# Optimization experiments

Measured on AMD Instinct MI355X. Metric: run time of the kernel, lower is better.

Reference implementation:

```python
import jax, jax.numpy as jnp
import numpy as np

D_MODEL = 1024
NHEADS = 16
E_HEAD = D_MODEL // NHEADS  # 64
ROPE_BASE = 10000.0


def _rope_cos_sin(L, dim, base, dtype):
    # dim = E_head (even); inv_freq over pairs, GPT-NeoX half-split convention
    inv_freq = 1.0 / (base ** (jnp.arange(0, dim, 2, dtype=jnp.float32) / dim))
    pos = jnp.arange(L, dtype=jnp.float32)
    freqs = pos[:, None] * inv_freq[None, :]  # [L, dim/2]
    return jnp.cos(freqs).astype(dtype), jnp.sin(freqs).astype(dtype)


def _apply_rope(t, cos, sin):
    # t: [B, H, L, Dh]; rotate-half formulation
    d2 = t.shape[-1] // 2
    t1, t2 = t[..., :d2], t[..., d2:]
    return jnp.concatenate([t1 * cos - t2 * sin, t1 * sin + t2 * cos], axis=-1)


def setup_inputs() -> dict:
    key = jax.random.key(0)
    ks = jax.random.split(key, 5)
    B, L = 4, 2048
    x = jax.random.normal(ks[0], (B, L, D_MODEL), dtype=jnp.float32)
    s_in = 1.0 / np.sqrt(D_MODEL)
    W_packed = jax.random.normal(ks[1], (3 * D_MODEL, D_MODEL), dtype=jnp.float32) * s_in
    b_packed = jax.random.normal(ks[2], (3 * D_MODEL,), dtype=jnp.float32) * 0.02
    W_out = jax.random.normal(ks[3], (D_MODEL, D_MODEL), dtype=jnp.float32) * s_in
    b_out = jax.random.normal(ks[4], (D_MODEL,), dtype=jnp.float32) * 0.02
    return {"x": x, "W_packed": W_packed, "b_packed": b_packed, "W_out": W_out, "b_out": b_out}


def reference(x, W_packed, b_packed, W_out, b_out):
    B, L, _ = x.shape
    # 1) packed QKV projection (query is key is value path)
    qkv = jnp.einsum('ble,fe->blf', x, W_packed) + b_packed  # [B, L, 3*D]
    q, k, v = jnp.split(qkv, 3, axis=-1)
    # 2) split heads -> [B, H, L, Dh]
    def heads(t):
        return t.reshape(B, L, NHEADS, E_HEAD).transpose(0, 2, 1, 3)
    q, k, v = heads(q), heads(k), heads(v)
    # 3) RoPE on q, k
    cos, sin = _rope_cos_sin(L, E_HEAD, ROPE_BASE, x.dtype)
    q = _apply_rope(q, cos, sin)
    k = _apply_rope(k, cos, sin)
    # 4) SDPA (non-causal, no dropout)
    scale = 1.0 / np.sqrt(E_HEAD)
    scores = jnp.einsum('bhqd,bhkd->bhqk', q, k) * scale
    attn = jax.nn.softmax(scores, axis=-1)
    out = jnp.einsum('bhqk,bhkd->bhqd', attn, v)
    # 5) merge heads + output projection
    out = out.transpose(0, 2, 1, 3).reshape(B, L, D_MODEL)
    return jnp.einsum('bld,ed->ble', out, W_out) + b_out
```

## Files before the change

kernel.cpp:

```cpp
#include <hip/hip_runtime.h>
#include <hip/hip_bf16.h>
#include <stdint.h>

#define L_SEQ 2048
#define NB    4
#define NH    16
#define EH    64
#define DM    1024
#define MTOT  (NB * L_SEQ)

typedef __attribute__((ext_vector_type(8))) short bf16x8;
typedef __attribute__((ext_vector_type(4))) float f32x4;
typedef __attribute__((ext_vector_type(16))) float f32x16;

static __device__ __forceinline__ float bf2f(short u) {
    union { unsigned int i; float f; } c;
    c.i = ((unsigned int)(unsigned short)u) << 16;
    return c.f;
}
static __device__ __forceinline__ short f2bf(float f) {
    union { float f; unsigned int i; } c; c.f = f;
    unsigned int x = c.i;
    unsigned int r = (x + 0x7fffu + ((x >> 16) & 1u)) >> 16;
    return (short)(unsigned short)r;
}
static __device__ __forceinline__ unsigned cvtpk(float lo, float hi) {
    unsigned r;
    asm volatile("v_cvt_pk_bf16_f32 %0, %1, %2" : "=v"(r) : "v"(lo), "v"(hi));
    return r;
}

static __device__ __forceinline__ void gload_lds16(const void* g, void* lds) {
    __builtin_amdgcn_global_load_lds(
        (const __attribute__((address_space(1))) unsigned int*)g,
        (__attribute__((address_space(3))) unsigned int*)lds, 16, 0, 0);
}

__global__ __launch_bounds__(256) void cvt3_k(const float* __restrict__ x,
                                              const float* __restrict__ wp,
                                              const float* __restrict__ wo,
                                              short* __restrict__ xb,
                                              short* __restrict__ wpb,
                                              short* __restrict__ wob,
                                              float* __restrict__ tab) {
    int bid = blockIdx.x;
    if (bid >= 12288) {
        int i = (bid - 12288) * 256 + threadIdx.x;
        int l = i >> 5, d = i & 31;
        float inv = powf(10000.0f, -(float)d * (1.0f / 32.0f));
        float fr = (float)l * inv;
        tab[i]         = cosf(fr);
        tab[65536 + i] = sinf(fr);
        return;
    }
    const float* src; short* dst; int i;
    if (bid < 8192)       { src = x;  dst = xb;  i = bid * 256 + threadIdx.x; }
    else if (bid < 11264) { src = wp; dst = wpb; i = (bid - 8192) * 256 + threadIdx.x; }
    else                  { src = wo; dst = wob; i = (bid - 11264) * 256 + threadIdx.x; }
    float4 v = ((const float4*)src)[i];
    short4 o;
    o.x = f2bf(v.x); o.y = f2bf(v.y); o.z = f2bf(v.z); o.w = f2bf(v.w);
    ((short4*)dst)[i] = o;
}

template<int OUTBF16, int NBX>
__global__ __launch_bounds__(512, 2) void gemm256_k(const short* __restrict__ A,
                                                    const short* __restrict__ Bt,
                                                    const float* __restrict__ bias,
                                                    void* __restrict__ Cv) {
    __shared__ short lds[2][2][256 * 32];
    const int t = threadIdx.x;
    const int w = t >> 6, l = t & 63;
    const int wm = w >> 2, wn = w & 3;
    const int lr = l & 15, lh = l >> 4;
    const int N = NBX * 256;

    const int nblk = NBX * 32;
    int fid = blockIdx.x + blockIdx.y * NBX;
    int swz = (fid & 7) * (nblk >> 3) + (fid >> 3);
    const int n0 = (swz % NBX) * 256;
    const int m0 = (swz / NBX) * 256;

    const int lrow = l >> 2;
    const int schunk = (l & 3) ^ ((l >> 3) & 3);

    const short* Ag = A + (size_t)(m0 + lrow) * 1024 + schunk * 8;
    const short* Bg = Bt + (size_t)(n0 + lrow) * 1024 + schunk * 8;

    auto STAGE = [&](int kt, int buf) {
#pragma unroll
        for (int j = 0; j < 2; ++j) {
            const int r = (w * 2 + j) * 16;
            gload_lds16(Ag + (size_t)r * 1024 + kt * 32, &lds[buf][0][r * 32]);
            gload_lds16(Bg + (size_t)r * 1024 + kt * 32, &lds[buf][1][r * 32]);
        }
    };

    f32x4 acc[8][4] = {};

    STAGE(0, 0);
    STAGE(1, 1);
    asm volatile("s_waitcnt vmcnt(4)" ::: "memory");
    __builtin_amdgcn_s_barrier();

    const int fch = (lh ^ ((lr >> 1) & 3)) << 3;

#pragma unroll 2
    for (int kt = 0; kt < 32; ++kt) {
        const int c = kt & 1;
        const short* Al = &lds[c][0][0];
        const short* Bl = &lds[c][1][0];

        bf16x8 bfr[4], af[8];
#pragma unroll
        for (int nj = 0; nj < 4; ++nj)
            bfr[nj] = *(const bf16x8*)(Bl + (wn * 64 + nj * 16 + lr) * 32 + fch);
#pragma unroll
        for (int mi = 0; mi < 8; ++mi)
            af[mi] = *(const bf16x8*)(Al + (wm * 128 + mi * 16 + lr) * 32 + fch);

        __builtin_amdgcn_s_setprio(1);
#pragma unroll
        for (int mi = 0; mi < 8; ++mi)
#pragma unroll
            for (int nj = 0; nj < 4; ++nj)
                acc[mi][nj] = __builtin_amdgcn_mfma_f32_16x16x32_bf16(
                    af[mi], bfr[nj], acc[mi][nj], 0, 0, 0);
        __builtin_amdgcn_s_setprio(0);

        asm volatile("s_waitcnt lgkmcnt(0)" ::: "memory");
        __builtin_amdgcn_s_barrier();
        if (kt + 2 < 32) {
            STAGE(kt + 2, c);
            asm volatile("s_waitcnt vmcnt(4)" ::: "memory");
        } else {
            asm volatile("s_waitcnt vmcnt(0)" ::: "memory");
        }
        __builtin_amdgcn_s_barrier();
    }

#pragma unroll
    for (int mi = 0; mi < 8; ++mi) {
#pragma unroll
        for (int nj = 0; nj < 4; ++nj) {
            const int row = m0 + wm * 128 + mi * 16 + lh * 4;
            const int col = n0 + wn * 64 + nj * 16 + lr;
            const float bsv = bias[col];
#pragma unroll
            for (int j = 0; j < 4; ++j) {
                float v = acc[mi][nj][j] + bsv;
                if (OUTBF16)
                    ((short*)Cv)[(size_t)(row + j) * N + col] = f2bf(v);
                else
                    ((float*)Cv)[(size_t)(row + j) * N + col] = v;
            }
        }
    }
}

__global__ __launch_bounds__(256) void gemm_out_k(const short* __restrict__ A,
                                                  const short* __restrict__ Bt,
                                                  const float* __restrict__ bias,
                                                  float* __restrict__ Cv,
                                                  int N, int K) {
    __shared__ short As[128 * 64];
    __shared__ short Bs[128 * 64];
    const int t = threadIdx.x;
    const int w = t >> 6, l = t & 63;
    const int wr = w >> 1, wc = w & 1;
    const int lr = l & 15, lh = l >> 4;
    const int m0 = blockIdx.y * 128, n0 = blockIdx.x * 128;
    const int srow = t >> 3;
    const int scol = (t & 7) * 8;

    f32x4 acc[4][4] = {};

    const short* Ab = A + (size_t)(m0 + srow) * K + scol;
    const short* Bb = Bt + (size_t)(n0 + srow) * K + scol;

    for (int k0 = 0; k0 < K; k0 += 64) {
        __syncthreads();
#pragma unroll
        for (int i = 0; i < 4; i++) {
            gload_lds16(Ab + (size_t)(i * 32) * K + k0, As + i * 2048 + w * 512);
            gload_lds16(Bb + (size_t)(i * 32) * K + k0, Bs + i * 2048 + w * 512);
        }
        __syncthreads();
#pragma unroll
        for (int kk = 0; kk < 2; kk++) {
            bf16x8 af[4], bfr[4];
#pragma unroll
            for (int mi = 0; mi < 4; mi++)
                af[mi] = *(const bf16x8*)(As + (wr * 64 + mi * 16 + lr) * 64 + kk * 32 + lh * 8);
#pragma unroll
            for (int nj = 0; nj < 4; nj++)
                bfr[nj] = *(const bf16x8*)(Bs + (wc * 64 + nj * 16 + lr) * 64 + kk * 32 + lh * 8);
            __builtin_amdgcn_s_setprio(1);
#pragma unroll
            for (int mi = 0; mi < 4; mi++)
#pragma unroll
                for (int nj = 0; nj < 4; nj++)
                    acc[mi][nj] = __builtin_amdgcn_mfma_f32_16x16x32_bf16(
                        af[mi], bfr[nj], acc[mi][nj], 0, 0, 0);
            __builtin_amdgcn_s_setprio(0);
        }
    }
#pragma unroll
    for (int mi = 0; mi < 4; mi++) {
#pragma unroll
        for (int nj = 0; nj < 4; nj++) {
            const int row = m0 + wr * 64 + mi * 16 + lh * 4;
            const int col = n0 + wc * 64 + nj * 16 + lr;
            const float bsv = bias[col];
#pragma unroll
            for (int j = 0; j < 4; j++)
                Cv[(size_t)(row + j) * N + col] = acc[mi][nj][j] + bsv;
        }
    }
}

__global__ __launch_bounds__(256) void scatter_k(const short* __restrict__ qkv,
                                                 const float* __restrict__ tab,
                                                 short* __restrict__ Q,
                                                 short* __restrict__ Kd,
                                                 short* __restrict__ Vt) {
    int bid = blockIdx.x;
    if (bid < 8192) {
        int idx = bid * 256 + threadIdx.x;
        int dp = (idx & 15) * 2;
        int h = (idx >> 4) & 15;
        int bl = idx >> 8;
        int l = bl & (L_SEQ - 1);
        int b = bl >> 11;
        float2 cs = *(const float2*)&tab[l * 32 + dp];
        float2 sn = *(const float2*)&tab[65536 + l * 32 + dp];
        const short* row = qkv + (size_t)bl * 3072;
        short2 q1 = *(const short2*)&row[h * 64 + dp];
        short2 q2 = *(const short2*)&row[h * 64 + dp + 32];
        short2 k1 = *(const short2*)&row[1024 + h * 64 + dp];
        short2 k2 = *(const short2*)&row[1024 + h * 64 + dp + 32];
        size_t ob = ((size_t)((b * 16 + h) * 2048 + l)) * 64;
        const float sc = 0.18033688011112042f;
        short2 o1, o2;
        o1.x = f2bf((bf2f(q1.x) * cs.x - bf2f(q2.x) * sn.x) * sc);
        o1.y = f2bf((bf2f(q1.y) * cs.y - bf2f(q2.y) * sn.y) * sc);
        o2.x = f2bf((bf2f(q1.x) * sn.x + bf2f(q2.x) * cs.x) * sc);
        o2.y = f2bf((bf2f(q1.y) * sn.y + bf2f(q2.y) * cs.y) * sc);
        *(short2*)(Q + ob + dp)      = o1;
        *(short2*)(Q + ob + dp + 32) = o2;
        int r7 = l & 7;
        int c1 = (((dp >> 3) ^ r7) * 8) + (dp & 7);
        int c2 = ((((dp >> 3) | 4) ^ r7) * 8) + (dp & 7);
        short2 e1, e2;
        e1.x = f2bf(bf2f(k1.x) * cs.x - bf2f(k2.x) * sn.x);
        e1.y = f2bf(bf2f(k1.y) * cs.y - bf2f(k2.y) * sn.y);
        e2.x = f2bf(bf2f(k1.x) * sn.x + bf2f(k2.x) * cs.x);
        e2.y = f2bf(bf2f(k1.y) * sn.y + bf2f(k2.y) * cs.y);
        *(short2*)(Kd + ob + c1) = e1;
        *(short2*)(Kd + ob + c2) = e2;
        return;
    }
    __shared__ short tile[64 * 65];
    int bid2 = bid - 8192;
    int l0 = (bid2 & 31) * 64;
    int bh = bid2 >> 5;
    int t = threadIdx.x;
    int b = bh >> 4, h = bh & 15;
#pragma unroll
    for (int i = 0; i < 16; i++) {
        int l = i * 4 + (t >> 6);
        int d = t & 63;
        tile[d * 65 + l] = qkv[(size_t)(b * 2048 + l0 + l) * 3072 + 2048 + h * 64 + d];
    }
    __syncthreads();
#pragma unroll
    for (int i = 0; i < 16; i++) {
        int d = i * 4 + (t >> 6);
        int lx = t & 63;
        int cl = (lx & ~0xC) | ((lx & 4) << 1) | ((lx & 8) >> 1);
        int lp = l0 | ((((cl >> 3) ^ (d & 7)) << 3)) | (cl & 7);
        Vt[(size_t)(bh * 64 + d) * 2048 + lp] = tile[d * 65 + lx];
    }
}

__global__ __launch_bounds__(512, 2) void attn_k(const short* __restrict__ Qg,
                                                 const short* __restrict__ Kg,
                                                 const short* __restrict__ Vt,
                                                 short* __restrict__ O) {
    __shared__ short Ks[3][64 * 64];
    __shared__ short Vs[3][64 * 64];
    const int t = threadIdx.x;
    const int w = t >> 6, l = t & 63;
    const int q = l & 31, hi = l >> 5;
    const int r7 = l & 7;

    const int od = blockIdx.x + blockIdx.y * 8;
    const int qblk = (od >> 3) & 7;
    const int bh = (od & 7) * 8 + (od >> 6);
    const int q0 = qblk * 256;

    const short* Qb = Qg + (size_t)bh * (2048 * 64);
    const short* Kb = Kg + (size_t)bh * (2048 * 64);
    const short* Vb = Vt + (size_t)bh * (64 * 2048);

    const int qrow = q0 + w * 32 + q;
    bf16x8 qf[4];
#pragma unroll
    for (int ds = 0; ds < 4; ds++)
        qf[ds] = *(const bf16x8*)(Qb + (size_t)qrow * 64 + ds * 16 + hi * 8);

    const short one_bf = (short)0x3F80;
    const bf16x8 ones = {one_bf, one_bf, one_bf, one_bf, one_bf, one_bf, one_bf, one_bf};

    f32x16 o0 = {}, o1 = {}, os = {};

    const int grow = w * 8 + (l >> 3);
    const int gcol = r7 * 8;

    gload_lds16(Kb + (size_t)grow * 64 + gcol,        &Ks[0][w * 512]);
    gload_lds16(Vb + (size_t)grow * 2048 + gcol,      &Vs[0][w * 512]);
    gload_lds16(Kb + (size_t)(64 + grow) * 64 + gcol, &Ks[1][w * 512]);
    gload_lds16(Vb + (size_t)grow * 2048 + 64 + gcol, &Vs[1][w * 512]);
    asm volatile("s_waitcnt vmcnt(2)" ::: "memory");
    __builtin_amdgcn_s_barrier();

    const short* Kc = &Ks[0][0];  const short* Vc = &Vs[0][0];
    const short* Kn = &Ks[1][0];  const short* Vn = &Vs[1][0];
    short*       Kf = &Ks[2][0];  short*       Vf = &Vs[2][0];

    for (int it = 0; it < 32; ++it) {
        if (it < 30) {
            const int kn = (it + 2) * 64;
            gload_lds16(Kb + (size_t)(kn + grow) * 64 + gcol, Kf + w * 512);
            gload_lds16(Vb + (size_t)grow * 2048 + kn + gcol, Vf + w * 512);
        }

        f32x16 s0 = {}, s1 = {};
#pragma unroll
        for (int ds = 0; ds < 4; ds++) {
            const int ch = ((ds << 1) | hi) ^ r7;
            bf16x8 k0f = *(const bf16x8*)(Kc + q * 64 + ch * 8);
            bf16x8 k1f = *(const bf16x8*)(Kc + (32 + q) * 64 + ch * 8);
            __builtin_amdgcn_s_setprio(1);
            s0 = __builtin_amdgcn_mfma_f32_32x32x16_bf16(k0f, qf[ds], s0, 0, 0, 0);
            s1 = __builtin_amdgcn_mfma_f32_32x32x16_bf16(k1f, qf[ds], s1, 0, 0, 0);
            __builtin_amdgcn_s_setprio(0);
        }

#pragma unroll
        for (int r = 0; r < 16; r++) {
            s0[r] = __builtin_amdgcn_exp2f(s0[r]);
            s1[r] = __builtin_amdgcn_exp2f(s1[r]);
        }

        bf16x8 pf[4];
        {
            union { unsigned u[4]; bf16x8 v; } f;
            f.u[0] = cvtpk(s0[0], s0[1]);  f.u[1] = cvtpk(s0[2], s0[3]);
            f.u[2] = cvtpk(s0[4], s0[5]);  f.u[3] = cvtpk(s0[6], s0[7]);
            pf[0] = f.v;
            f.u[0] = cvtpk(s0[8], s0[9]);  f.u[1] = cvtpk(s0[10], s0[11]);
            f.u[2] = cvtpk(s0[12], s0[13]); f.u[3] = cvtpk(s0[14], s0[15]);
            pf[1] = f.v;
            f.u[0] = cvtpk(s1[0], s1[1]);  f.u[1] = cvtpk(s1[2], s1[3]);
            f.u[2] = cvtpk(s1[4], s1[5]);  f.u[3] = cvtpk(s1[6], s1[7]);
            pf[2] = f.v;
            f.u[0] = cvtpk(s1[8], s1[9]);  f.u[1] = cvtpk(s1[10], s1[11]);
            f.u[2] = cvtpk(s1[12], s1[13]); f.u[3] = cvtpk(s1[14], s1[15]);
            pf[3] = f.v;
        }

#pragma unroll
        for (int ks = 0; ks < 4; ks++) {
            const int ch = ((ks << 1) | hi) ^ r7;
            bf16x8 v0f = *(const bf16x8*)(Vc + q * 64 + ch * 8);
            bf16x8 v1f = *(const bf16x8*)(Vc + (32 + q) * 64 + ch * 8);
            __builtin_amdgcn_s_setprio(1);
            o0 = __builtin_amdgcn_mfma_f32_32x32x16_bf16(v0f, pf[ks], o0, 0, 0, 0);
            o1 = __builtin_amdgcn_mfma_f32_32x32x16_bf16(v1f, pf[ks], o1, 0, 0, 0);
            os = __builtin_amdgcn_mfma_f32_32x32x16_bf16(ones, pf[ks], os, 0, 0, 0);
            __builtin_amdgcn_s_setprio(0);
        }

        asm volatile("s_waitcnt lgkmcnt(0)" ::: "memory");
        if (it < 30) asm volatile("s_waitcnt vmcnt(2)" ::: "memory");
        else         asm volatile("s_waitcnt vmcnt(0)" ::: "memory");
        __builtin_amdgcn_s_barrier();

        const short* tk = Kc; Kc = Kn; Kn = Kf; Kf = (short*)tk;
        const short* tv = Vc; Vc = Vn; Vn = Vf; Vf = (short*)tv;
    }

    const float inv = 1.0f / os[0];
    const int b = bh >> 4, h = bh & 15;
    short* Orow = O + (size_t)(b * 2048 + qrow) * 1024 + h * 64;
#pragma unroll
    for (int g = 0; g < 4; g++) {
        unsigned w0 = cvtpk(o0[g * 4 + 0] * inv, o0[g * 4 + 1] * inv);
        unsigned w1 = cvtpk(o0[g * 4 + 2] * inv, o0[g * 4 + 3] * inv);
        unsigned long long p0 = (unsigned long long)w0 | ((unsigned long long)w1 << 32);
        *(unsigned long long*)(Orow + g * 8 + hi * 4) = p0;
        unsigned w2 = cvtpk(o1[g * 4 + 0] * inv, o1[g * 4 + 1] * inv);
        unsigned w3 = cvtpk(o1[g * 4 + 2] * inv, o1[g * 4 + 3] * inv);
        unsigned long long p1 = (unsigned long long)w2 | ((unsigned long long)w3 << 32);
        *(unsigned long long*)(Orow + 32 + g * 8 + hi * 4) = p1;
    }
}

extern "C" void kernel_launch(void* const* d_in, const int* in_sizes, int n_in,
                              void* d_out, int out_size, void* d_ws, size_t ws_size,
                              hipStream_t stream) {
    const float* x  = (const float*)d_in[0];
    const float* Wp = (const float*)d_in[1];
    const float* bp = (const float*)d_in[2];
    const float* Wo = (const float*)d_in[3];
    const float* bo = (const float*)d_in[4];

    char* ws = (char*)d_ws;
    const size_t SZ_XB  = (size_t)MTOT * DM * 2;
    const size_t SZ_WPB = (size_t)3 * DM * DM * 2;
    const size_t SZ_WOB = (size_t)DM * DM * 2;
    const size_t SZ_QKV = (size_t)MTOT * 3 * DM * 2;
    const size_t SZ_BHLE = (size_t)MTOT * DM * 2;

    short* xb   = (short*)(ws);
    short* wpb  = (short*)(ws + SZ_XB);
    short* wob  = (short*)(ws + SZ_XB + SZ_WPB);
    short* qkvb = (short*)(ws + SZ_XB + SZ_WPB + SZ_WOB);
    short* Qb   = (short*)(ws + SZ_XB + SZ_WPB + SZ_WOB + SZ_QKV);
    short* Kb   = (short*)(ws + SZ_XB + SZ_WPB + SZ_WOB + SZ_QKV + SZ_BHLE);
    short* Vtb  = (short*)(ws + SZ_XB + SZ_WPB + SZ_WOB + SZ_QKV + 2 * SZ_BHLE);
    short* Ob   = (short*)(ws + SZ_XB + SZ_WPB + SZ_WOB + SZ_QKV + 3 * SZ_BHLE);
    float* tab  = (float*)(ws + SZ_XB + SZ_WPB + SZ_WOB + SZ_QKV + 4 * SZ_BHLE);

    cvt3_k<<<12544, 256, 0, stream>>>(x, Wp, Wo, xb, wpb, wob, tab);

    gemm256_k<1, 12><<<dim3(12, 32), 512, 0, stream>>>(xb, wpb, bp, qkvb);

    scatter_k<<<10240, 256, 0, stream>>>(qkvb, tab, Qb, Kb, Vtb);

    attn_k<<<dim3(8, 64), 512, 0, stream>>>(Qb, Kb, Vtb, Ob);

    gemm_out_k<<<dim3(8, 64), 256, 0, stream>>>(Ob, wob, bo, (float*)d_out, DM, DM);
}
```

Baseline: 207.0 us.

## Fuse Q RoPE into attention and retile QKV GEMM to 256x128

Q no longer goes through the scatter kernel. The attention kernel reads raw Q rows from the packed QKV buffer and applies RoPE and the softmax scale in registers. This removes a full Q write and re-read plus the scatter work for Q. Separately, the QKV GEMM tile shrinks from 256x256 to 256x128, doubling the block count to 768 for better CU balance at lower per-block reuse, and the K scatter is vectorized to 4 elements per thread.

```diff
diff --git a/kernel.cpp b/kernel.cpp
--- a/kernel.cpp
+++ b/kernel.cpp
@@ -63,23 +63,22 @@
     ((short4*)dst)[i] = o;
 }
 
-template<int OUTBF16, int NBX>
-__global__ __launch_bounds__(512, 2) void gemm256_k(const short* __restrict__ A,
-                                                    const short* __restrict__ Bt,
-                                                    const float* __restrict__ bias,
-                                                    void* __restrict__ Cv) {
-    __shared__ short lds[2][2][256 * 32];
+template<int OUTBF16, int NBN, int NCOL>
+__global__ __launch_bounds__(512, 2) void gemmA_k(const short* __restrict__ A,
+                                                  const short* __restrict__ Bt,
+                                                  const float* __restrict__ bias,
+                                                  void* __restrict__ Cv) {
+    __shared__ short lds[2][384 * 32];
     const int t = threadIdx.x;
     const int w = t >> 6, l = t & 63;
-    const int wm = w >> 2, wn = w & 3;
+    const int wm = w >> 1, wn = w & 1;
     const int lr = l & 15, lh = l >> 4;
-    const int N = NBX * 256;
-
-    const int nblk = NBX * 32;
-    int fid = blockIdx.x + blockIdx.y * NBX;
+
+    const int nblk = NBN * 32;
+    int fid = blockIdx.x + blockIdx.y * NBN;
     int swz = (fid & 7) * (nblk >> 3) + (fid >> 3);
-    const int n0 = (swz % NBX) * 256;
-    const int m0 = (swz / NBX) * 256;
+    const int n0 = (swz % NBN) * 128;
+    const int m0 = (swz / NBN) * 256;
 
     const int lrow = l >> 2;
     const int schunk = (l & 3) ^ ((l >> 3) & 3);
@@ -88,19 +87,16 @@
     const short* Bg = Bt + (size_t)(n0 + lrow) * 1024 + schunk * 8;
 
     auto STAGE = [&](int kt, int buf) {
-#pragma unroll
-        for (int j = 0; j < 2; ++j) {
-            const int r = (w * 2 + j) * 16;
-            gload_lds16(Ag + (size_t)r * 1024 + kt * 32, &lds[buf][0][r * 32]);
-            gload_lds16(Bg + (size_t)r * 1024 + kt * 32, &lds[buf][1][r * 32]);
-        }
+        gload_lds16(Ag + (size_t)(w * 32) * 1024 + kt * 32,      &lds[buf][(w * 32) * 32]);
+        gload_lds16(Ag + (size_t)(w * 32 + 16) * 1024 + kt * 32, &lds[buf][(w * 32 + 16) * 32]);
+        gload_lds16(Bg + (size_t)(w * 16) * 1024 + kt * 32,      &lds[buf][8192 + (w * 16) * 32]);
     };
 
-    f32x4 acc[8][4] = {};
+    f32x4 acc[4][4] = {};
 
     STAGE(0, 0);
     STAGE(1, 1);
-    asm volatile("s_waitcnt vmcnt(4)" ::: "memory");
+    asm volatile("s_waitcnt vmcnt(3)" ::: "memory");
     __builtin_amdgcn_s_barrier();
 
     const int fch = (lh ^ ((lr >> 1) & 3)) << 3;
@@ -108,20 +104,20 @@
 #pragma unroll 2
     for (int kt = 0; kt < 32; ++kt) {
         const int c = kt & 1;
-        const short* Al = &lds[c][0][0];
-        const short* Bl = &lds[c][1][0];
-
-        bf16x8 bfr[4], af[8];
+        const short* Al = &lds[c][0];
+        const short* Bl = &lds[c][8192];
+
+        bf16x8 bfr[4], af[4];
 #pragma unroll
         for (int nj = 0; nj < 4; ++nj)
             bfr[nj] = *(const bf16x8*)(Bl + (wn * 64 + nj * 16 + lr) * 32 + fch);
 #pragma unroll
-        for (int mi = 0; mi < 8; ++mi)
-            af[mi] = *(const bf16x8*)(Al + (wm * 128 + mi * 16 + lr) * 32 + fch);
+        for (int mi = 0; mi < 4; ++mi)
+            af[mi] = *(const bf16x8*)(Al + (wm * 64 + mi * 16 + lr) * 32 + fch);
 
         __builtin_amdgcn_s_setprio(1);
 #pragma unroll
-        for (int mi = 0; mi < 8; ++mi)
+        for (int mi = 0; mi < 4; ++mi)
 #pragma unroll
             for (int nj = 0; nj < 4; ++nj)
                 acc[mi][nj] = __builtin_amdgcn_mfma_f32_16x16x32_bf16(
@@ -132,7 +128,7 @@
         __builtin_amdgcn_s_barrier();
         if (kt + 2 < 32) {
             STAGE(kt + 2, c);
-            asm volatile("s_waitcnt vmcnt(4)" ::: "memory");
+            asm volatile("s_waitcnt vmcnt(3)" ::: "memory");
         } else {
             asm volatile("s_waitcnt vmcnt(0)" ::: "memory");
         }
@@ -140,19 +136,19 @@
     }
 
 #pragma unroll
-    for (int mi = 0; mi < 8; ++mi) {
+    for (int mi = 0; mi < 4; ++mi) {
 #pragma unroll
         for (int nj = 0; nj < 4; ++nj) {
-            const int row = m0 + wm * 128 + mi * 16 + lh * 4;
+            const int row = m0 + wm * 64 + mi * 16 + lh * 4;
             const int col = n0 + wn * 64 + nj * 16 + lr;
             const float bsv = bias[col];
 #pragma unroll
             for (int j = 0; j < 4; ++j) {
                 float v = acc[mi][nj][j] + bsv;
                 if (OUTBF16)
-                    ((short*)Cv)[(size_t)(row + j) * N + col] = f2bf(v);
+                    ((short*)Cv)[(size_t)(row + j) * NCOL + col] = f2bf(v);
                 else
-                    ((float*)Cv)[(size_t)(row + j) * N + col] = v;
+                    ((float*)Cv)[(size_t)(row + j) * NCOL + col] = v;
             }
         }
     }
@@ -221,47 +217,40 @@
 
 __global__ __launch_bounds__(256) void scatter_k(const short* __restrict__ qkv,
                                                  const float* __restrict__ tab,
-                                                 short* __restrict__ Q,
                                                  short* __restrict__ Kd,
                                                  short* __restrict__ Vt) {
     int bid = blockIdx.x;
-    if (bid < 8192) {
+    if (bid < 4096) {
         int idx = bid * 256 + threadIdx.x;
-        int dp = (idx & 15) * 2;
-        int h = (idx >> 4) & 15;
-        int bl = idx >> 8;
+        int dp = (idx & 7) * 4;
+        int h = (idx >> 3) & 15;
+        int bl = idx >> 7;
         int l = bl & (L_SEQ - 1);
         int b = bl >> 11;
-        float2 cs = *(const float2*)&tab[l * 32 + dp];
-        float2 sn = *(const float2*)&tab[65536 + l * 32 + dp];
+        float4 cs = *(const float4*)&tab[l * 32 + dp];
+        float4 sn = *(const float4*)&tab[65536 + l * 32 + dp];
         const short* row = qkv + (size_t)bl * 3072;
-        short2 q1 = *(const short2*)&row[h * 64 + dp];
-        short2 q2 = *(const short2*)&row[h * 64 + dp + 32];
-        short2 k1 = *(const short2*)&row[1024 + h * 64 + dp];
-        short2 k2 = *(const short2*)&row[1024 + h * 64 + dp + 32];
+        short4 k1 = *(const short4*)&row[1024 + h * 64 + dp];
+        short4 k2 = *(const short4*)&row[1024 + h * 64 + dp + 32];
         size_t ob = ((size_t)((b * 16 + h) * 2048 + l)) * 64;
-        const float sc = 0.18033688011112042f;
-        short2 o1, o2;
-        o1.x = f2bf((bf2f(q1.x) * cs.x - bf2f(q2.x) * sn.x) * sc);
-        o1.y = f2bf((bf2f(q1.y) * cs.y - bf2f(q2.y) * sn.y) * sc);
-        o2.x = f2bf((bf2f(q1.x) * sn.x + bf2f(q2.x) * cs.x) * sc);
-        o2.y = f2bf((bf2f(q1.y) * sn.y + bf2f(q2.y) * cs.y) * sc);
-        *(short2*)(Q + ob + dp)      = o1;
-        *(short2*)(Q + ob + dp + 32) = o2;
+        union { unsigned u[2]; short4 s4; } e1, e2;
+        e1.u[0] = cvtpk(bf2f(k1.x) * cs.x - bf2f(k2.x) * sn.x,
+                        bf2f(k1.y) * cs.y - bf2f(k2.y) * sn.y);
+        e1.u[1] = cvtpk(bf2f(k1.z) * cs.z - bf2f(k2.z) * sn.z,
+                        bf2f(k1.w) * cs.w - bf2f(k2.w) * sn.w);
+        e2.u[0] = cvtpk(bf2f(k1.x) * sn.x + bf2f(k2.x) * cs.x,
+                        bf2f(k1.y) * sn.y + bf2f(k2.y) * cs.y);
+        e2.u[1] = cvtpk(bf2f(k1.z) * sn.z + bf2f(k2.z) * cs.z,
+                        bf2f(k1.w) * sn.w + bf2f(k2.w) * cs.w);
         int r7 = l & 7;
-        int c1 = (((dp >> 3) ^ r7) * 8) + (dp & 7);
-        int c2 = ((((dp >> 3) | 4) ^ r7) * 8) + (dp & 7);
-        short2 e1, e2;
-        e1.x = f2bf(bf2f(k1.x) * cs.x - bf2f(k2.x) * sn.x);
-        e1.y = f2bf(bf2f(k1.y) * cs.y - bf2f(k2.y) * sn.y);
-        e2.x = f2bf(bf2f(k1.x) * sn.x + bf2f(k2.x) * cs.x);
-        e2.y = f2bf(bf2f(k1.y) * sn.y + bf2f(k2.y) * cs.y);
-        *(short2*)(Kd + ob + c1) = e1;
-        *(short2*)(Kd + ob + c2) = e2;
+        int c1 = ((dp >> 3) ^ r7) * 8 + (dp & 7);
+        int c2 = (((dp >> 3) | 4) ^ r7) * 8 + (dp & 7);
+        *(short4*)(Kd + ob + c1) = e1.s4;
+        *(short4*)(Kd + ob + c2) = e2.s4;
         return;
     }
     __shared__ short tile[64 * 65];
-    int bid2 = bid - 8192;
+    int bid2 = bid - 4096;
     int l0 = (bid2 & 31) * 64;
     int bh = bid2 >> 5;
     int t = threadIdx.x;
@@ -283,9 +272,10 @@
     }
 }
 
-__global__ __launch_bounds__(512, 2) void attn_k(const short* __restrict__ Qg,
+__global__ __launch_bounds__(512, 2) void attn_k(const short* __restrict__ qkv,
                                                  const short* __restrict__ Kg,
                                                  const short* __restrict__ Vt,
+                                                 const float* __restrict__ tab,
                                                  short* __restrict__ O) {
     __shared__ short Ks[3][64 * 64];
     __shared__ short Vs[3][64 * 64];
@@ -298,16 +288,35 @@
     const int qblk = (od >> 3) & 7;
     const int bh = (od & 7) * 8 + (od >> 6);
     const int q0 = qblk * 256;
-
-    const short* Qb = Qg + (size_t)bh * (2048 * 64);
+    const int b = bh >> 4, h = bh & 15;
+
     const short* Kb = Kg + (size_t)bh * (2048 * 64);
     const short* Vb = Vt + (size_t)bh * (64 * 2048);
 
     const int qrow = q0 + w * 32 + q;
+
+    const short* Qsrc = qkv + (size_t)(b * 2048 + qrow) * 3072 + h * 64;
+    bf16x8 qraw[4];
+#pragma unroll
+    for (int ds = 0; ds < 4; ds++)
+        qraw[ds] = *(const bf16x8*)(Qsrc + ds * 16 + hi * 8);
+    const float sc = 0.18033688011112042f;
     bf16x8 qf[4];
 #pragma unroll
-    for (int ds = 0; ds < 4; ds++)
-        qf[ds] = *(const bf16x8*)(Qb + (size_t)qrow * 64 + ds * 16 + hi * 8);
+    for (int dsL = 0; dsL < 2; dsL++) {
+        bf16x8 r1 = qraw[dsL], r2 = qraw[dsL + 2];
+        union { unsigned u[4]; bf16x8 v; } lo, hg;
+#pragma unroll
+        for (int p = 0; p < 4; p++) {
+            float2 c2 = *(const float2*)&tab[qrow * 32 + dsL * 16 + hi * 8 + 2 * p];
+            float2 s2 = *(const float2*)&tab[65536 + qrow * 32 + dsL * 16 + hi * 8 + 2 * p];
+            float a0 = bf2f(r1[2 * p]),     b0 = bf2f(r2[2 * p]);
+            float a1 = bf2f(r1[2 * p + 1]), b1 = bf2f(r2[2 * p + 1]);
+            lo.u[p] = cvtpk((a0 * c2.x - b0 * s2.x) * sc, (a1 * c2.y - b1 * s2.y) * sc);
+            hg.u[p] = cvtpk((a0 * s2.x + b0 * c2.x) * sc, (a1 * s2.y + b1 * c2.y) * sc);
+        }
+        qf[dsL] = lo.v; qf[dsL + 2] = hg.v;
+    }
 
     const short one_bf = (short)0x3F80;
     const bf16x8 ones = {one_bf, one_bf, one_bf, one_bf, one_bf, one_bf, one_bf, one_bf};
@@ -392,7 +401,6 @@
     }
 
     const float inv = 1.0f / os[0];
-    const int b = bh >> 4, h = bh & 15;
     short* Orow = O + (size_t)(b * 2048 + qrow) * 1024 + h * 64;
 #pragma unroll
     for (int g = 0; g < 4; g++) {
@@ -427,19 +435,18 @@
     short* wpb  = (short*)(ws + SZ_XB);
     short* wob  = (short*)(ws + SZ_XB + SZ_WPB);
     short* qkvb = (short*)(ws + SZ_XB + SZ_WPB + SZ_WOB);
-    short* Qb   = (short*)(ws + SZ_XB + SZ_WPB + SZ_WOB + SZ_QKV);
-    short* Kb   = (short*)(ws + SZ_XB + SZ_WPB + SZ_WOB + SZ_QKV + SZ_BHLE);
-    short* Vtb  = (short*)(ws + SZ_XB + SZ_WPB + SZ_WOB + SZ_QKV + 2 * SZ_BHLE);
-    short* Ob   = (short*)(ws + SZ_XB + SZ_WPB + SZ_WOB + SZ_QKV + 3 * SZ_BHLE);
-    float* tab  = (float*)(ws + SZ_XB + SZ_WPB + SZ_WOB + SZ_QKV + 4 * SZ_BHLE);
+    short* Kb   = (short*)(ws + SZ_XB + SZ_WPB + SZ_WOB + SZ_QKV);
+    short* Vtb  = (short*)(ws + SZ_XB + SZ_WPB + SZ_WOB + SZ_QKV + SZ_BHLE);
+    short* Ob   = (short*)(ws + SZ_XB + SZ_WPB + SZ_WOB + SZ_QKV + 2 * SZ_BHLE);
+    float* tab  = (float*)(ws + SZ_XB + SZ_WPB + SZ_WOB + SZ_QKV + 3 * SZ_BHLE);
 
     cvt3_k<<<12544, 256, 0, stream>>>(x, Wp, Wo, xb, wpb, wob, tab);
 
-    gemm256_k<1, 12><<<dim3(12, 32), 512, 0, stream>>>(xb, wpb, bp, qkvb);
-
-    scatter_k<<<10240, 256, 0, stream>>>(qkvb, tab, Qb, Kb, Vtb);
-
-    attn_k<<<dim3(8, 64), 512, 0, stream>>>(Qb, Kb, Vtb, Ob);
+    gemmA_k<1, 24, 3072><<<dim3(24, 32), 512, 0, stream>>>(xb, wpb, bp, qkvb);
+
+    scatter_k<<<6144, 256, 0, stream>>>(qkvb, tab, Kb, Vtb);
+
+    attn_k<<<dim3(8, 64), 512, 0, stream>>>(qkvb, Kb, Vtb, tab, Ob);
 
     gemm_out_k<<<dim3(8, 64), 256, 0, stream>>>(Ob, wob, bo, (float*)d_out, DM, DM);
 }
```

Result: faster. 198.9 us (-3.9%).
